# Kernel tuning notes

Measured on AMD Instinct MI355X. Metric: run time of the kernel, lower is better.

The kernel has to match this reference:

```python
import jax, jax.numpy as jnp
import numpy as np

S, B, D, N, DH = 1024, 2, 1024, 16, 64  # seq, batch, d_model, n_head, d_head
EPS = 1e-5


def setup_inputs() -> dict:
    key = jax.random.key(0)
    k0, k1, k2, k3 = jax.random.split(key, 4)
    h = jax.random.normal(k0, (S, B, D), dtype=jnp.float32)
    Wq = jax.random.normal(k1, (N * DH, D), dtype=jnp.float32) * 0.02
    Wkv = jax.random.normal(k2, (2 * N * DH, D), dtype=jnp.float32) * 0.02
    Wo = jax.random.normal(k3, (D, N * DH), dtype=jnp.float32) * 0.02
    gamma = jnp.ones((D,), dtype=jnp.float32)
    beta = jnp.zeros((D,), dtype=jnp.float32)
    return {"h": h, "Wq": Wq, "Wkv": Wkv, "Wo": Wo, "gamma": gamma, "beta": beta}


def reference(h, Wq, Wkv, Wo, gamma, beta):
    scale = 1.0 / np.sqrt(DH).astype(np.float32)
    # projections (torch Linear: x @ W.T), no mems so c == h
    q = (h @ Wq.T).reshape(S, B, N, DH)
    kv = h @ Wkv.T                      # [S,B,2*N*DH]
    k, v = jnp.split(kv, 2, axis=-1)
    k = k.reshape(S, B, N, DH)
    v = v.reshape(S, B, N, DH)
    # full attention scores [i,j,b,n]
    score = jnp.einsum('ibnd,jbnd->ijbn', q, k) * scale
    prob = jax.nn.softmax(score, axis=1)  # softmax over keys j
    # twicing correction (layer_num >= 14): P <- 2P - P @ P per (b,n)
    p = prob.transpose(2, 3, 0, 1)       # [b,n,i,j]
    p = 2.0 * p - jnp.matmul(p, p)
    prob = p.transpose(2, 3, 0, 1)       # back to [i,j,b,n]
    # attention output
    vec = jnp.einsum('ijbn,jbnd->ibnd', prob, v).reshape(S, B, N * DH)
    attn_out = vec @ Wo.T                # [S,B,D]
    # post-LN residual
    x = h + attn_out
    mu = jnp.mean(x, axis=-1, keepdims=True)
    var = jnp.mean(jnp.square(x - mu), axis=-1, keepdims=True)
    return (x - mu) / jnp.sqrt(var + EPS) * gamma + beta
```

## Files before the change

### kernel.cpp

```cpp
#include <hip/hip_runtime.h>

typedef unsigned short u16;
typedef unsigned int u32;
typedef __attribute__((ext_vector_type(8))) short short8;
typedef __attribute__((ext_vector_type(4))) float f32x4;

constexpr int kN = 16, kDH = 64, kD = 1024;
constexpr float kEps = 1e-5f;

__device__ __forceinline__ u16 f2b(float f) {
  u32 u = __float_as_uint(f);
  u += 0x7fffu + ((u >> 16) & 1u);
  return (u16)(u >> 16);
}
__device__ __forceinline__ float b2f(u32 bits) {
  return __uint_as_float(bits << 16);
}

__device__ __forceinline__ void gload16(const u16* g, u16* l) {
  __builtin_amdgcn_global_load_lds(
      (const __attribute__((address_space(1))) void*)g,
      (__attribute__((address_space(3))) void*)l, 16, 0, 0);
}

__device__ __forceinline__ short8 read8sw(const u16* base, int row, int colel) {
  return *(const short8*)(base + (row << 6) + (colel ^ ((row & 7) << 3)));
}

__device__ __forceinline__ int permS(int s) {
  return (s & ~31) + ((s & 12) << 1) + ((s & 16) >> 2) + (s & 3);
}

__global__ __launch_bounds__(256) void cvt_all(const float* __restrict__ h,
                                               const float* __restrict__ wq,
                                               const float* __restrict__ wkv,
                                               const float* __restrict__ wo,
                                               u16* __restrict__ hb, u16* __restrict__ wqb,
                                               u16* __restrict__ wkvb, u16* __restrict__ wob) {
  long idx = (long)blockIdx.x * 256 + threadIdx.x;
  const float* in;
  u16* out;
  long base;
  if (idx < 524288L) { in = h; out = hb; base = idx; }
  else if (idx < 786432L) { in = wq; out = wqb; base = idx - 524288L; }
  else if (idx < 1310720L) { in = wkv; out = wkvb; base = idx - 786432L; }
  else { in = wo; out = wob; base = idx - 1310720L; }
  float4 v = *(const float4*)(in + base * 4);
  uint2 o;
  o.x = (u32)f2b(v.x) | ((u32)f2b(v.y) << 16);
  o.y = (u32)f2b(v.z) | ((u32)f2b(v.w) << 16);
  *(uint2*)(out + base * 4) = o;
}

struct GemmParams {
  const u16* A; long ldA;
  const u16* B; long ldB;
  const u16* B2;
  int K;
  u16* ob; float* of; long ldO;
  u16* ob2;
  u16* aux_b16;
};

template <int MODE>
__global__ __launch_bounds__(256) void gemm_tile(GemmParams p) {
  __shared__ __align__(16) u16 sm[2][8192];
  const int tid = threadIdx.x, lane = tid & 63, w = tid >> 6;
  const int wR = w >> 1, wC = w & 1;
  const int lr = lane & 15, lk = lane >> 4;
  const int bm0 = blockIdx.y * 64, bn0 = blockIdx.x * 64;
  const int m0 = bm0 + wR * 32, n0 = bn0 + wC * 32;
  const u16* A = p.A;
  const u16* B = (MODE == 6 && bn0 >= 1024) ? (p.B2 - 1048576) : p.B;

  f32x4 acc[2][2] = {};

  auto stage = [&](int k0, int buf) {
#pragma unroll
    for (int i = 0; i < 4; ++i) {
      const int cbase = i * 256 + w * 64;
      const int c = cbase + lane;
      const int row = c >> 3;
      const int col = ((c & 7) ^ (row & 7)) * 8;
      const u16* g;
      if (cbase < 512) {
        g = A + (long)(bm0 + row) * p.ldA + k0 + col;
      } else {
        g = B + (long)(bn0 + (row - 64)) * p.ldB + k0 + col;
      }
      gload16(g, &sm[buf][(size_t)c * 8]);
    }
  };

  auto compute = [&](int buf) {
    const u16* As = sm[buf];
    const u16* Bs = sm[buf] + 4096;
    short8 af[2][2], bf[2][2];
#pragma unroll
    for (int mi = 0; mi < 2; ++mi)
#pragma unroll
      for (int kk = 0; kk < 2; ++kk) {
        af[mi][kk] = read8sw(As, (wR * 2 + mi) * 16 + lr, kk * 32 + lk * 8);
        bf[mi][kk] = read8sw(Bs, (wC * 2 + mi) * 16 + lr, kk * 32 + lk * 8);
      }
#pragma unroll
    for (int kk = 0; kk < 2; ++kk)
#pragma unroll
      for (int mi = 0; mi < 2; ++mi)
#pragma unroll
        for (int ni = 0; ni < 2; ++ni)
          acc[mi][ni] = __builtin_amdgcn_mfma_f32_16x16x32_bf16(af[mi][kk], bf[ni][kk], acc[mi][ni], 0, 0, 0);
  };

  const int nt = p.K / 64;
  stage(0, 0);
  __syncthreads();
  for (int t = 0; t < nt - 1; ++t) {
    stage((t + 1) * 64, (t & 1) ^ 1);
    compute(t & 1);
    __syncthreads();
  }
  compute((nt - 1) & 1);

#pragma unroll
  for (int mi = 0; mi < 2; ++mi)
#pragma unroll
    for (int ni = 0; ni < 2; ++ni)
#pragma unroll
      for (int r = 0; r < 4; ++r) {
        int row = m0 + mi * 16 + lk * 4 + r;
        int col = n0 + ni * 16 + lr;
        float v = acc[mi][ni][r];
        if constexpr (MODE == 6) {
          if (col < 1024) {
            p.ob[(long)row * 1024 + col] = f2b(v);
          } else if (col < 2048) {
            p.ob2[(long)row * 1024 + (col - 1024)] = f2b(v);
          } else {
            int c = col - 2048, n = c >> 6, dd = c & 63, s = row >> 1, b = row & 1;
            p.aux_b16[(((long)((b * kN + n) * kDH + dd)) << 10) + permS(s)] = f2b(v);
          }
        } else {
          p.of[(long)row * p.ldO + col] = v;
        }
      }
}

template <bool PASS1>
__global__ __launch_bounds__(256, 4) void flash_tw(const u16* __restrict__ qp,
                                                   const u16* __restrict__ kp,
                                                   const u16* __restrict__ bp,
                                                   float* __restrict__ linv_g,
                                                   u16* __restrict__ outp) {
  __shared__ __align__(16) u16 Ks[2][64 * 64];
  __shared__ __align__(16) u16 Bs[2][64 * 64];
  __shared__ float lred[64], lrinv[64];
  const int z = blockIdx.y, qb0 = blockIdx.x * 64;
  const int tid = threadIdx.x, lane = tid & 63, w = tid >> 6;
  const int lr = lane & 15, lk = lane >> 4;
  const int q0 = w * 16;

  auto stageKB = [&](int j, int buf) {
#pragma unroll
    for (int i = 0; i < 2; ++i) {
      int c = i * 256 + w * 64 + lane;
      int row = c >> 3, col = (c & 7) ^ (row & 7);
      gload16(kp + (long)(j * 64 + row) * 2048 + z * 64 + col * 8, Ks[buf] + c * 8);
      gload16(bp + (long)z * 65536 + (long)row * 1024 + j * 64 + col * 8, Bs[buf] + c * 8);
    }
  };

  short8 qf[2];
#pragma unroll
  for (int kk = 0; kk < 2; ++kk)
    qf[kk] = *(const short8*)(qp + (long)(qb0 + q0 + lr) * 2048 + z * 64 + kk * 32 + lk * 8);

  stageKB(0, 0);
  __syncthreads();

  f32x4 acc[4] = {};
  float lsum = 0.f;

  for (int j = 0; j < 16; ++j) {
    const int cur = j & 1;
    if (j < 15) stageKB(j + 1, cur ^ 1);
    f32x4 st[4];
#pragma unroll
    for (int kt = 0; kt < 4; ++kt) st[kt] = (f32x4){0.f, 0.f, 0.f, 0.f};
#pragma unroll
    for (int kk = 0; kk < 2; ++kk)
#pragma unroll
      for (int kt = 0; kt < 4; ++kt) {
        short8 kf = read8sw(Ks[cur], kt * 16 + lr, kk * 32 + lk * 8);
        st[kt] = __builtin_amdgcn_mfma_f32_16x16x32_bf16(kf, qf[kk], st[kt], 0, 0, 0);
      }
    uint2 pk[4];
#pragma unroll
    for (int kt = 0; kt < 4; ++kt) {
      float e0 = __expf(st[kt][0] * 0.125f);
      float e1 = __expf(st[kt][1] * 0.125f);
      float e2 = __expf(st[kt][2] * 0.125f);
      float e3 = __expf(st[kt][3] * 0.125f);
      if (PASS1) lsum += e0 + e1 + e2 + e3;
      pk[kt].x = (u32)f2b(e0) | ((u32)f2b(e1) << 16);
      pk[kt].y = (u32)f2b(e2) | ((u32)f2b(e3) << 16);
    }
#pragma unroll
    for (int kk = 0; kk < 2; ++kk) {
      union { u32 u[4]; short8 s8; } pa;
      pa.u[0] = pk[kk * 2].x; pa.u[1] = pk[kk * 2].y;
      pa.u[2] = pk[kk * 2 + 1].x; pa.u[3] = pk[kk * 2 + 1].y;
#pragma unroll
      for (int dt = 0; dt < 4; ++dt) {
        short8 bf = read8sw(Bs[cur], dt * 16 + lr, kk * 32 + lk * 8);
        acc[dt] = __builtin_amdgcn_mfma_f32_16x16x32_bf16(pa.s8, bf, acc[dt], 0, 0, 0);
      }
    }
    __syncthreads();
  }

  float iv[4];
  if (PASS1) {
    lsum += __shfl_xor(lsum, 16);
    lsum += __shfl_xor(lsum, 32);
    if (lane < 16) lred[q0 + lr] = lsum;
    __syncthreads();
    if (tid < 64) {
      float v = 1.f / lred[tid];
      lrinv[tid] = v;
      linv_g[(long)z * 1024 + qb0 + tid] = v;
    }
    __syncthreads();
#pragma unroll
    for (int r = 0; r < 4; ++r) iv[r] = lrinv[q0 + lk * 4 + r];
  } else {
    float4 l4 = *(const float4*)(linv_g + (long)z * 1024 + qb0 + q0 + lk * 4);
    iv[0] = l4.x; iv[1] = l4.y; iv[2] = l4.z; iv[3] = l4.w;
  }

  const int sq = qb0 + q0 + lk * 4;
  const int sp = (sq & ~31) + ((sq & 12) << 1) + ((sq & 16) >> 2);
#pragma unroll
  for (int dt = 0; dt < 4; ++dt) {
    const int d = dt * 16 + lr;
    if (PASS1) {
      uint2 o_;
      o_.x = (u32)f2b(acc[dt][0] * iv[0]) | ((u32)f2b(acc[dt][1] * iv[1]) << 16);
      o_.y = (u32)f2b(acc[dt][2] * iv[2]) | ((u32)f2b(acc[dt][3] * iv[3]) << 16);
      *(uint2*)(outp + (long)z * 65536 + (long)d * 1024 + sp) = o_;
    } else {
      uint2 ut = *(const uint2*)(bp + (long)z * 65536 + (long)d * 1024 + sp);
      float u0 = b2f(ut.x & 0xffffu), u1 = b2f(ut.x >> 16);
      float u2 = b2f(ut.y & 0xffffu), u3 = b2f(ut.y >> 16);
      long ob = (long)sq * 2048 + z * 64 + d;
      outp[ob]        = f2b(2.f * u0 - acc[dt][0] * iv[0]);
      outp[ob + 2048] = f2b(2.f * u1 - acc[dt][1] * iv[1]);
      outp[ob + 4096] = f2b(2.f * u2 - acc[dt][2] * iv[2]);
      outp[ob + 6144] = f2b(2.f * u3 - acc[dt][3] * iv[3]);
    }
  }
}

__global__ __launch_bounds__(256) void resid_ln(const float* __restrict__ h,
                                                const float* __restrict__ attn,
                                                const float* __restrict__ gamma,
                                                const float* __restrict__ beta,
                                                float* __restrict__ out) {
  __shared__ float rs[4], rs2[4];
  const long row = blockIdx.x;
  const int t = threadIdx.x;
  long base = (row << 10) + t * 4;
  float4 hv = *(const float4*)(h + base);
  float4 av = *(const float4*)(attn + base);
  float x0 = hv.x + av.x, x1 = hv.y + av.y, x2 = hv.z + av.z, x3 = hv.w + av.w;
  float s = x0 + x1 + x2 + x3;
  float s2 = x0 * x0 + x1 * x1 + x2 * x2 + x3 * x3;
  for (int o = 32; o; o >>= 1) { s += __shfl_xor(s, o); s2 += __shfl_xor(s2, o); }
  int wid = t >> 6;
  if ((t & 63) == 0) { rs[wid] = s; rs2[wid] = s2; }
  __syncthreads();
  s = rs[0] + rs[1] + rs[2] + rs[3];
  s2 = rs2[0] + rs2[1] + rs2[2] + rs2[3];
  float mean = s * (1.f / 1024.f);
  float var = s2 * (1.f / 1024.f) - mean * mean;
  float rstd = rsqrtf(var + kEps);
  int d = t * 4;
  float4 g = *(const float4*)(gamma + d);
  float4 bt = *(const float4*)(beta + d);
  float4 o_;
  o_.x = (x0 - mean) * rstd * g.x + bt.x;
  o_.y = (x1 - mean) * rstd * g.y + bt.y;
  o_.z = (x2 - mean) * rstd * g.z + bt.z;
  o_.w = (x3 - mean) * rstd * g.w + bt.w;
  *(float4*)(out + base) = o_;
}

extern "C" void kernel_launch(void* const* d_in, const int* in_sizes, int n_in,
                              void* d_out, int out_size, void* d_ws, size_t ws_size,
                              hipStream_t stream) {
  const float* h = (const float*)d_in[0];
  const float* Wq = (const float*)d_in[1];
  const float* Wkv = (const float*)d_in[2];
  const float* Wo = (const float*)d_in[3];
  const float* gamma = (const float*)d_in[4];
  const float* beta = (const float*)d_in[5];
  float* out = (float*)d_out;

  char* ws = (char*)d_ws;
  size_t off = 0;
  auto alloc = [&](size_t bytes) -> void* {
    void* p = ws + off;
    off = (off + bytes + 255) & ~(size_t)255;
    return p;
  };
  u16* hb = (u16*)alloc(2097152ULL * 2);
  u16* Wqb = (u16*)alloc(1048576ULL * 2);
  u16* Wkvb = (u16*)alloc(2097152ULL * 2);
  u16* Wob = (u16*)alloc(1048576ULL * 2);
  u16* qb = (u16*)alloc(2097152ULL * 2);
  u16* kb = (u16*)alloc(2097152ULL * 2);
  u16* vtb = (u16*)alloc(2097152ULL * 2);
  u16* Ut = (u16*)alloc(2097152ULL * 2);
  float* linv = (float*)alloc(32768ULL * 4);
  u16* vecb = (u16*)alloc(2097152ULL * 2);
  float* attn = (float*)alloc(2097152ULL * 4);
  (void)ws_size; (void)n_in; (void)in_sizes; (void)out_size;

  cvt_all<<<6144, 256, 0, stream>>>(h, Wq, Wkv, Wo, hb, Wqb, Wkvb, Wob);

  {
    GemmParams p{};
    p.A = hb; p.ldA = 1024;
    p.B = Wqb; p.ldB = 1024; p.B2 = Wkvb;
    p.K = 1024; p.ob = qb; p.ob2 = kb; p.aux_b16 = vtb;
    gemm_tile<6><<<dim3(48, 32, 1), 256, 0, stream>>>(p);
  }
  flash_tw<true><<<dim3(16, 32), 256, 0, stream>>>(qb, kb, vtb, linv, Ut);
  flash_tw<false><<<dim3(16, 32), 256, 0, stream>>>(qb, kb, Ut, linv, vecb);
  {
    GemmParams p{};
    p.A = vecb; p.ldA = 1024;
    p.B = Wob; p.ldB = 1024;
    p.K = 1024; p.of = attn; p.ldO = 1024;
    gemm_tile<5><<<dim3(16, 32, 1), 256, 0, stream>>>(p);
  }
  resid_ln<<<2048, 256, 0, stream>>>(h, attn, gamma, beta, out);
}
```

Before: 99.54 us.

## Issue loads two tiles ahead with explicit vmcnt waits in GEMM and attention

Both the GEMM tile kernel and the flash-style attention kernel now prefetch two K-steps ahead into the double buffer. Each iteration waits on a partial vmcnt, so only the oldest tile's async global-to-LDS loads must have landed, instead of calling __syncthreads, which drains everything. Raw s_barrier plus lgkmcnt waits protect buffer reuse. The attention exp is rewritten as exp2f with a folded scale constant. This deepens overlap of memory with MFMA work, but the hand-written waitcnt counts (vmcnt(4)) must exactly match the number of loads issued per stage, or data races appear.

Result: faster. 94.85 us (-4.7%).

```diff
diff --git a/kernel.cpp b/kernel.cpp
--- a/kernel.cpp
+++ b/kernel.cpp
@@ -7,6 +7,7 @@
 
 constexpr int kN = 16, kDH = 64, kD = 1024;
 constexpr float kEps = 1e-5f;
+constexpr float kExp2Scale = 0.18033688011112042f;
 
 __device__ __forceinline__ u16 f2b(float f) {
   u32 u = __float_as_uint(f);
@@ -21,6 +22,19 @@
   __builtin_amdgcn_global_load_lds(
       (const __attribute__((address_space(1))) void*)g,
       (__attribute__((address_space(3))) void*)l, 16, 0, 0);
+}
+
+__device__ __forceinline__ void wait_vm4() {
+  asm volatile("s_waitcnt vmcnt(4)" ::: "memory");
+  __builtin_amdgcn_sched_barrier(0);
+}
+__device__ __forceinline__ void wait_vm0() {
+  asm volatile("s_waitcnt vmcnt(0)" ::: "memory");
+  __builtin_amdgcn_sched_barrier(0);
+}
+__device__ __forceinline__ void wait_lgkm0() {
+  asm volatile("s_waitcnt lgkmcnt(0)" ::: "memory");
+  __builtin_amdgcn_sched_barrier(0);
 }
 
 __device__ __forceinline__ short8 read8sw(const u16* base, int row, int colel) {
@@ -78,12 +92,11 @@
   auto stage = [&](int k0, int buf) {
 #pragma unroll
     for (int i = 0; i < 4; ++i) {
-      const int cbase = i * 256 + w * 64;
-      const int c = cbase + lane;
+      const int c = i * 256 + w * 64 + lane;
       const int row = c >> 3;
       const int col = ((c & 7) ^ (row & 7)) * 8;
       const u16* g;
-      if (cbase < 512) {
+      if (row < 64) {
         g = A + (long)(bm0 + row) * p.ldA + k0 + col;
       } else {
         g = B + (long)(bn0 + (row - 64)) * p.ldB + k0 + col;
@@ -114,13 +127,15 @@
 
   const int nt = p.K / 64;
   stage(0, 0);
-  __syncthreads();
-  for (int t = 0; t < nt - 1; ++t) {
-    stage((t + 1) * 64, (t & 1) ^ 1);
+  stage(64, 1);
+  for (int t = 0; t < nt; ++t) {
+    if (t < nt - 1) wait_vm4(); else wait_vm0();
+    __builtin_amdgcn_s_barrier();
     compute(t & 1);
-    __syncthreads();
-  }
-  compute((nt - 1) & 1);
+    wait_lgkm0();
+    __builtin_amdgcn_s_barrier();
+    if (t + 2 < nt) stage((t + 2) * 64, t & 1);
+  }
 
 #pragma unroll
   for (int mi = 0; mi < 2; ++mi)
@@ -160,6 +175,11 @@
   const int lr = lane & 15, lk = lane >> 4;
   const int q0 = w * 16;
 
+  short8 qf[2];
+#pragma unroll
+  for (int kk = 0; kk < 2; ++kk)
+    qf[kk] = *(const short8*)(qp + (long)(qb0 + q0 + lr) * 2048 + z * 64 + kk * 32 + lk * 8);
+
   auto stageKB = [&](int j, int buf) {
 #pragma unroll
     for (int i = 0; i < 2; ++i) {
@@ -169,21 +189,16 @@
       gload16(bp + (long)z * 65536 + (long)row * 1024 + j * 64 + col * 8, Bs[buf] + c * 8);
     }
   };
-
-  short8 qf[2];
-#pragma unroll
-  for (int kk = 0; kk < 2; ++kk)
-    qf[kk] = *(const short8*)(qp + (long)(qb0 + q0 + lr) * 2048 + z * 64 + kk * 32 + lk * 8);
-
   stageKB(0, 0);
-  __syncthreads();
+  stageKB(1, 1);
 
   f32x4 acc[4] = {};
   float lsum = 0.f;
 
   for (int j = 0; j < 16; ++j) {
     const int cur = j & 1;
-    if (j < 15) stageKB(j + 1, cur ^ 1);
+    if (j < 15) wait_vm4(); else wait_vm0();
+    __builtin_amdgcn_s_barrier();
     f32x4 st[4];
 #pragma unroll
     for (int kt = 0; kt < 4; ++kt) st[kt] = (f32x4){0.f, 0.f, 0.f, 0.f};
@@ -197,10 +212,10 @@
     uint2 pk[4];
 #pragma unroll
     for (int kt = 0; kt < 4; ++kt) {
-      float e0 = __expf(st[kt][0] * 0.125f);
-      float e1 = __expf(st[kt][1] * 0.125f);
-      float e2 = __expf(st[kt][2] * 0.125f);
-      float e3 = __expf(st[kt][3] * 0.125f);
+      float e0 = exp2f(st[kt][0] * kExp2Scale);
+      float e1 = exp2f(st[kt][1] * kExp2Scale);
+      float e2 = exp2f(st[kt][2] * kExp2Scale);
+      float e3 = exp2f(st[kt][3] * kExp2Scale);
       if (PASS1) lsum += e0 + e1 + e2 + e3;
       pk[kt].x = (u32)f2b(e0) | ((u32)f2b(e1) << 16);
       pk[kt].y = (u32)f2b(e2) | ((u32)f2b(e3) << 16);
@@ -216,7 +231,9 @@
         acc[dt] = __builtin_amdgcn_mfma_f32_16x16x32_bf16(pa.s8, bf, acc[dt], 0, 0, 0);
       }
     }
-    __syncthreads();
+    wait_lgkm0();
+    __builtin_amdgcn_s_barrier();
+    if (j < 14) stageKB(j + 2, cur);
   }
 
   float iv[4];
```
